# Optimization experiments

Hardware: AMD Instinct MI355X
Metric: run time of the kernel (lower is better)

## Reference

```python
import jax, jax.numpy as jnp
import numpy as np

B, T, D, H = 2, 2048, 1024, 16
DH = D // H


def setup_inputs() -> dict:
    key = jax.random.key(0)
    k1, k2, k3, k4 = jax.random.split(key, 4)
    x = jax.random.normal(k1, (B, T, D), dtype=jnp.float32)
    k = jax.random.normal(k2, (B, H, T, DH), dtype=jnp.float32)
    v = jax.random.normal(k3, (B, H, T, DH), dtype=jnp.float32)
    Wq = jax.random.normal(k4, (D, D), dtype=jnp.float32) * (1.0 / np.sqrt(D))
    return {"x": x, "k": k, "v": v, "Wq": Wq}


def reference(x, k, v, Wq):
    b, t, d = x.shape
    h = k.shape[1]
    scale = 1.0 / jnp.sqrt(jnp.float32(d))  # note: sqrt(d), NOT sqrt(d/h), per source
    # q = Linear(d, d, bias=False): y = x @ Wq.T, then split into heads
    q = jnp.einsum('btd,ed->bte', x, Wq).reshape(b, t, h, -1).transpose(0, 2, 1, 3)  # [b,h,t,dh]
    scores = jnp.einsum('bhqd,bhkd->bhqk', q, k) * scale  # [b,h,t,t]
    causal = jnp.triu(jnp.ones((t, t), dtype=bool), k=1)  # True above diagonal -> masked
    scores = jnp.where(causal[None, None], -jnp.inf, scores)
    a = jax.nn.softmax(scores, axis=-1)
    out = jnp.einsum('bhqk,bhkd->bhqd', a, v).transpose(0, 2, 1, 3).reshape(b, t, d)
    return x + out
```

## Files before the change

kernel.cpp:

```cpp
#include <hip/hip_runtime.h>
#include <hip/hip_bf16.h>

#define B_ 2
#define T_ 2048
#define D_ 1024
#define H_ 16
#define DH_ 64

typedef __attribute__((ext_vector_type(8))) short bf16x8;
typedef __attribute__((ext_vector_type(4))) short bf16x4;
typedef __attribute__((ext_vector_type(4))) float f32x4;
typedef __attribute__((ext_vector_type(8))) unsigned short u16x8;

__device__ __forceinline__ unsigned short f2bf(float f) {
    unsigned int u = __float_as_uint(f);
    return (unsigned short)((u + 0x7FFFu + ((u >> 16) & 1u)) >> 16);
}

__device__ __forceinline__ void pack8(const float4& a, const float4& b, u16x8& o) {
    o[0] = f2bf(a.x); o[1] = f2bf(a.y); o[2] = f2bf(a.z); o[3] = f2bf(a.w);
    o[4] = f2bf(b.x); o[5] = f2bf(b.y); o[6] = f2bf(b.z); o[7] = f2bf(b.w);
}

__device__ __forceinline__ f32x4 mfma16(bf16x4 a, bf16x4 b, f32x4 c) {
#if defined(__HIP_DEVICE_COMPILE__)
    return __builtin_amdgcn_mfma_f32_16x16x16bf16_1k(a, b, c, 0, 0, 0);
#else
    return c;
#endif
}

__global__ __launch_bounds__(256) void conv_kernel(
    const float* __restrict__ k, const float* __restrict__ v,
    unsigned short* __restrict__ kb, unsigned short* __restrict__ vt)
{
    __shared__ float Ts[64][65];
    const int tid = threadIdx.x;
    const int bi = blockIdx.x;

    if (bi < 512) {
        const float* src = k + ((size_t)bi * 256 + tid) * 32;
        unsigned short* dst = kb + ((size_t)bi * 256 + tid) * 32;
        #pragma unroll
        for (int u = 0; u < 4; ++u) {
            const float4 a = *(const float4*)(src + u * 8);
            const float4 b = *(const float4*)(src + u * 8 + 4);
            u16x8 o; pack8(a, b, o);
            *(u16x8*)(dst + u * 8) = o;
        }
        return;
    }

    const int idx = bi - 512;
    const int t0 = (idx & 31) * 64;
    const int hb = idx >> 5;
    const size_t bh = (size_t)(hb >> 4) * H_ + (hb & 15);
    #pragma unroll
    for (int u = 0; u < 4; ++u) {
        const int tr = u * 16 + (tid >> 4);
        const int dc = (tid & 15) * 4;
        const float4 r = *(const float4*)(v + (bh * T_ + t0 + tr) * DH_ + dc);
        Ts[tr][dc + 0] = r.x; Ts[tr][dc + 1] = r.y;
        Ts[tr][dc + 2] = r.z; Ts[tr][dc + 3] = r.w;
    }
    __syncthreads();
    #pragma unroll
    for (int u = 0; u < 4; ++u) {
        const int dh = u * 16 + (tid >> 4);
        const int tc = (tid & 15) * 4;
        ushort4 o;
        o.x = f2bf(Ts[tc + 0][dh]); o.y = f2bf(Ts[tc + 1][dh]);
        o.z = f2bf(Ts[tc + 2][dh]); o.w = f2bf(Ts[tc + 3][dh]);
        *(ushort4*)(vt + (bh * DH_ + dh) * T_ + t0 + tc) = o;
    }
}

__global__ __launch_bounds__(256, 4) void mega_attn(
    const float* __restrict__ xg,
    const float* __restrict__ Wq,
    const unsigned short* __restrict__ kb,
    const unsigned short* __restrict__ vt,
    float* __restrict__ out)
{
    __shared__ __align__(16) char lds_raw[36864];
    unsigned short (*Ks0)[72] = (unsigned short(*)[72])(lds_raw);
    unsigned short (*Ks1)[72] = (unsigned short(*)[72])(lds_raw + 9216);
    unsigned short (*Vs0)[72] = (unsigned short(*)[72])(lds_raw + 18432);
    unsigned short (*Vs1)[72] = (unsigned short(*)[72])(lds_raw + 27648);
    unsigned short (*Ws)[72] = (unsigned short(*)[72])(lds_raw);
    unsigned short (*Xs)[72] = (unsigned short(*)[72])(lds_raw + 9216);
    unsigned short (*Qs)[72] = (unsigned short(*)[72])(lds_raw + 27648);

    const int tid = threadIdx.x;
    const int lane = tid & 63;
    const int w = tid >> 6;
    const int l15 = lane & 15, l4 = lane >> 4;
    const int bi = blockIdx.x;
    const int qt = 31 - (bi >> 5);
    const int hb = bi & 31;
    const int h = hb & 15, b = hb >> 4;
    const int q0 = qt * 64;
    const size_t bh = (size_t)b * H_ + h;

    {
        const int row = tid >> 2;
        const int cf  = (tid & 3) * 16;
        const float* xg0 = xg + ((size_t)b * T_ + q0 + row) * D_ + cf;
        const float* wg0 = Wq + (size_t)(h * 64 + row) * D_ + cf;

        f32x4 acc[4] = {};
        for (int k0 = 0; k0 < D_; k0 += 64) {
            {
                const float* g = xg0 + k0;
                u16x8 p0, p1;
                pack8(*(const float4*)(g), *(const float4*)(g + 4), p0);
                pack8(*(const float4*)(g + 8), *(const float4*)(g + 12), p1);
                *(u16x8*)&Xs[row][cf] = p0;
                *(u16x8*)&Xs[row][cf + 8] = p1;
                const float* gw = wg0 + k0;
                pack8(*(const float4*)(gw), *(const float4*)(gw + 4), p0);
                pack8(*(const float4*)(gw + 8), *(const float4*)(gw + 12), p1);
                *(u16x8*)&Ws[row][cf] = p0;
                *(u16x8*)&Ws[row][cf + 8] = p1;
            }
            __syncthreads();
            #pragma unroll
            for (int kc = 0; kc < 2; ++kc) {
                const bf16x8 wf = *(const bf16x8*)&Ws[w * 16 + l15][kc * 32 + l4 * 8];
                #pragma unroll
                for (int nt = 0; nt < 4; ++nt) {
                    const bf16x8 xf = *(const bf16x8*)&Xs[nt * 16 + l15][kc * 32 + l4 * 8];
                    acc[nt] = __builtin_amdgcn_mfma_f32_16x16x32_bf16(wf, xf, acc[nt], 0, 0, 0);
                }
            }
            __syncthreads();
        }
        const float qscale = 1.0f / 32.0f;
        #pragma unroll
        for (int nt = 0; nt < 4; ++nt) {
            ushort4 o;
            o.x = f2bf(acc[nt][0] * qscale); o.y = f2bf(acc[nt][1] * qscale);
            o.z = f2bf(acc[nt][2] * qscale); o.w = f2bf(acc[nt][3] * qscale);
            *(ushort4*)&Qs[nt * 16 + l15][w * 16 + l4 * 4] = o;
        }
    }
    __syncthreads();

    bf16x8 qf[2];
    #pragma unroll
    for (int kc = 0; kc < 2; ++kc)
        qf[kc] = *(const bf16x8*)&Qs[w * 16 + l15][kc * 32 + l4 * 8];

    f32x4 o_acc[4] = {};
    float m_i = -INFINITY, l_i = 0.0f;

    const int srow = tid >> 2;
    const int scol = (tid & 3) * 16;

    {
        const unsigned short* gk = kb + (bh * T_ + srow) * DH_ + scol;
        *(uint4*)&Ks0[srow][scol] = *(const uint4*)gk;
        *(uint4*)&Ks0[srow][scol + 8] = *(const uint4*)(gk + 8);
        const unsigned short* gv = vt + (bh * DH_ + srow) * T_ + scol;
        *(uint4*)&Vs0[srow][scol] = *(const uint4*)gv;
        *(uint4*)&Vs0[srow][scol + 8] = *(const uint4*)(gv + 8);
    }
    __syncthreads();

    int p = 0;
    for (int j0 = 0; j0 <= q0; j0 += 64) {
        unsigned short (*Ksp)[72] = p ? Ks1 : Ks0;
        unsigned short (*Vsp)[72] = p ? Vs1 : Vs0;
        unsigned short (*Ksn)[72] = p ? Ks0 : Ks1;
        unsigned short (*Vsn)[72] = p ? Vs0 : Vs1;

        const int jn = (j0 + 64 <= q0) ? j0 + 64 : 0;
        uint4 kr0, kr1, vr0, vr1;
        {
            const unsigned short* gk = kb + (bh * T_ + jn + srow) * DH_ + scol;
            kr0 = *(const uint4*)gk;
            kr1 = *(const uint4*)(gk + 8);
            const unsigned short* gv = vt + (bh * DH_ + srow) * T_ + jn + scol;
            vr0 = *(const uint4*)gv;
            vr1 = *(const uint4*)(gv + 8);
        }

        f32x4 st[4] = {};
        #pragma unroll
        for (int kc = 0; kc < 2; ++kc) {
            #pragma unroll
            for (int nt = 0; nt < 4; ++nt) {
                const bf16x8 kf = *(const bf16x8*)&Ksp[nt * 16 + l15][kc * 32 + l4 * 8];
                st[nt] = __builtin_amdgcn_mfma_f32_16x16x32_bf16(kf, qf[kc], st[nt], 0, 0, 0);
            }
        }

        if (j0 == q0) {
            const int thr = w * 16 + l15 - l4 * 4;
            #pragma unroll
            for (int nt = 0; nt < 4; ++nt)
                #pragma unroll
                for (int r = 0; r < 4; ++r)
                    if (nt * 16 + r > thr) st[nt][r] = -INFINITY;
        }

        float rm = -INFINITY;
        #pragma unroll
        for (int nt = 0; nt < 4; ++nt)
            #pragma unroll
            for (int r = 0; r < 4; ++r) rm = fmaxf(rm, st[nt][r]);
        rm = fmaxf(rm, __shfl_xor(rm, 16));
        rm = fmaxf(rm, __shfl_xor(rm, 32));
        const float mn = fmaxf(m_i, rm);
        const float alpha = __expf(m_i - mn);
        float rs = 0.0f;
        #pragma unroll
        for (int nt = 0; nt < 4; ++nt)
            #pragma unroll
            for (int r = 0; r < 4; ++r) {
                const float pv = __expf(st[nt][r] - mn);
                st[nt][r] = pv;
                rs += pv;
            }
        rs += __shfl_xor(rs, 16);
        rs += __shfl_xor(rs, 32);
        l_i = l_i * alpha + rs;
        m_i = mn;
        #pragma unroll
        for (int mt = 0; mt < 4; ++mt)
            #pragma unroll
            for (int r = 0; r < 4; ++r) o_acc[mt][r] *= alpha;

        bf16x4 pf[4];
        #pragma unroll
        for (int nt = 0; nt < 4; ++nt) {
            union { unsigned int u[2]; bf16x4 s; } cv;
            cv.u[0] = __builtin_amdgcn_perm(__float_as_uint(st[nt][1]),
                                            __float_as_uint(st[nt][0]), 0x07060302u);
            cv.u[1] = __builtin_amdgcn_perm(__float_as_uint(st[nt][3]),
                                            __float_as_uint(st[nt][2]), 0x07060302u);
            pf[nt] = cv.s;
        }

        #pragma unroll
        for (int c = 0; c < 4; ++c) {
            #pragma unroll
            for (int mt = 0; mt < 4; ++mt) {
                const bf16x4 vf = *(const bf16x4*)&Vsp[mt * 16 + l15][c * 16 + l4 * 4];
                o_acc[mt] = mfma16(vf, pf[c], o_acc[mt]);
            }
        }

        *(uint4*)&Ksn[srow][scol] = kr0;
        *(uint4*)&Ksn[srow][scol + 8] = kr1;
        *(uint4*)&Vsn[srow][scol] = vr0;
        *(uint4*)&Vsn[srow][scol + 8] = vr1;
        __syncthreads();
        p ^= 1;
    }

    const float inv = 1.0f / l_i;
    const int qrow = q0 + w * 16 + l15;
    #pragma unroll
    for (int mt = 0; mt < 4; ++mt) {
        #pragma unroll
        for (int r = 0; r < 4; ++r) {
            const int d = h * DH_ + mt * 16 + l4 * 4 + r;
            const size_t off = ((size_t)b * T_ + qrow) * D_ + d;
            out[off] = xg[off] + o_acc[mt][r] * inv;
        }
    }
}

extern "C" void kernel_launch(void* const* d_in, const int* in_sizes, int n_in,
                              void* d_out, int out_size, void* d_ws, size_t ws_size,
                              hipStream_t stream) {
    const float* x  = (const float*)d_in[0];
    const float* k  = (const float*)d_in[1];
    const float* v  = (const float*)d_in[2];
    const float* Wq = (const float*)d_in[3];
    float* out = (float*)d_out;

    const size_t NE = (size_t)B_ * H_ * T_ * DH_;
    unsigned short* kb = (unsigned short*)d_ws;
    unsigned short* vt = kb + NE;

    conv_kernel<<<1536, 256, 0, stream>>>(k, v, kb, vt);
    mega_attn<<<1024, 256, 0, stream>>>(x, Wq, kb, vt, out);
}
```

Baseline: 169.2 us.

## Pre-convert x and Wq to bf16 and double-buffer the Q projection loop

The preprocessing kernel now also converts x and Wq to bf16 in workspace, so the fused attention kernel loads half-width data for its Q projection and skips repeated fp32-to-bf16 conversion. Each Wq head slice is loaded by 32 blocks and each x row tile by 16, so converting once removes redundant conversion and fp32 traffic. The Q-projection k-loop becomes register-prefetched and double-buffered in LDS, with one barrier per iteration instead of two. The cost is an extra pass writing bf16 copies of x and Wq plus more workspace, and the conversion kernel grows.

```diff
diff --git a/kernel.cpp b/kernel.cpp
--- a/kernel.cpp
+++ b/kernel.cpp
@@ -32,15 +32,23 @@
 
 __global__ __launch_bounds__(256) void conv_kernel(
     const float* __restrict__ k, const float* __restrict__ v,
-    unsigned short* __restrict__ kb, unsigned short* __restrict__ vt)
+    const float* __restrict__ x, const float* __restrict__ Wq,
+    unsigned short* __restrict__ kb, unsigned short* __restrict__ vt,
+    unsigned short* __restrict__ xb, unsigned short* __restrict__ wqb)
 {
     __shared__ float Ts[64][65];
     const int tid = threadIdx.x;
     const int bi = blockIdx.x;
 
-    if (bi < 512) {
-        const float* src = k + ((size_t)bi * 256 + tid) * 32;
-        unsigned short* dst = kb + ((size_t)bi * 256 + tid) * 32;
+    if (bi < 1152) {
+        const float* src;
+        unsigned short* dst;
+        if (bi < 512)       { src = k  + ((size_t)bi * 256 + tid) * 32;
+                              dst = kb  + ((size_t)bi * 256 + tid) * 32; }
+        else if (bi < 1024) { src = x  + ((size_t)(bi - 512) * 256 + tid) * 32;
+                              dst = xb  + ((size_t)(bi - 512) * 256 + tid) * 32; }
+        else                { src = Wq + ((size_t)(bi - 1024) * 256 + tid) * 32;
+                              dst = wqb + ((size_t)(bi - 1024) * 256 + tid) * 32; }
         #pragma unroll
         for (int u = 0; u < 4; ++u) {
             const float4 a = *(const float4*)(src + u * 8);
@@ -51,7 +59,7 @@
         return;
     }
 
-    const int idx = bi - 512;
+    const int idx = bi - 1152;
     const int t0 = (idx & 31) * 64;
     const int hb = idx >> 5;
     const size_t bh = (size_t)(hb >> 4) * H_ + (hb & 15);
@@ -76,20 +84,23 @@
 }
 
 __global__ __launch_bounds__(256, 4) void mega_attn(
-    const float* __restrict__ xg,
-    const float* __restrict__ Wq,
+    const unsigned short* __restrict__ xb,
+    const unsigned short* __restrict__ wqb,
     const unsigned short* __restrict__ kb,
     const unsigned short* __restrict__ vt,
+    const float* __restrict__ xg,
     float* __restrict__ out)
 {
     __shared__ __align__(16) char lds_raw[36864];
+    unsigned short (*Ws0)[72] = (unsigned short(*)[72])(lds_raw);
+    unsigned short (*Xs0)[72] = (unsigned short(*)[72])(lds_raw + 9216);
+    unsigned short (*Ws1)[72] = (unsigned short(*)[72])(lds_raw + 18432);
+    unsigned short (*Xs1)[72] = (unsigned short(*)[72])(lds_raw + 27648);
+    unsigned short (*Qs)[72]  = (unsigned short(*)[72])(lds_raw + 27648);
     unsigned short (*Ks0)[72] = (unsigned short(*)[72])(lds_raw);
     unsigned short (*Ks1)[72] = (unsigned short(*)[72])(lds_raw + 9216);
     unsigned short (*Vs0)[72] = (unsigned short(*)[72])(lds_raw + 18432);
     unsigned short (*Vs1)[72] = (unsigned short(*)[72])(lds_raw + 27648);
-    unsigned short (*Ws)[72] = (unsigned short(*)[72])(lds_raw);
-    unsigned short (*Xs)[72] = (unsigned short(*)[72])(lds_raw + 9216);
-    unsigned short (*Qs)[72] = (unsigned short(*)[72])(lds_raw + 27648);
 
     const int tid = threadIdx.x;
     const int lane = tid & 63;
@@ -102,39 +113,59 @@
     const int q0 = qt * 64;
     const size_t bh = (size_t)b * H_ + h;
 
+    const int srow = tid >> 2;
+    const int scol = (tid & 3) * 16;
+
+    f32x4 acc[4] = {};
     {
-        const int row = tid >> 2;
-        const int cf  = (tid & 3) * 16;
-        const float* xg0 = xg + ((size_t)b * T_ + q0 + row) * D_ + cf;
-        const float* wg0 = Wq + (size_t)(h * 64 + row) * D_ + cf;
-
-        f32x4 acc[4] = {};
-        for (int k0 = 0; k0 < D_; k0 += 64) {
-            {
-                const float* g = xg0 + k0;
-                u16x8 p0, p1;
-                pack8(*(const float4*)(g), *(const float4*)(g + 4), p0);
-                pack8(*(const float4*)(g + 8), *(const float4*)(g + 12), p1);
-                *(u16x8*)&Xs[row][cf] = p0;
-                *(u16x8*)&Xs[row][cf + 8] = p1;
-                const float* gw = wg0 + k0;
-                pack8(*(const float4*)(gw), *(const float4*)(gw + 4), p0);
-                pack8(*(const float4*)(gw + 8), *(const float4*)(gw + 12), p1);
-                *(u16x8*)&Ws[row][cf] = p0;
-                *(u16x8*)&Ws[row][cf + 8] = p1;
-            }
-            __syncthreads();
+        const unsigned short* xg0 = xb  + ((size_t)b * T_ + q0 + srow) * D_ + scol;
+        const unsigned short* wg0 = wqb + (size_t)(h * 64 + srow) * D_ + scol;
+
+        uint4 xr0 = *(const uint4*)(xg0);
+        uint4 xr1 = *(const uint4*)(xg0 + 8);
+        uint4 wr0 = *(const uint4*)(wg0);
+        uint4 wr1 = *(const uint4*)(wg0 + 8);
+        *(uint4*)&Xs0[srow][scol] = xr0;
+        *(uint4*)&Xs0[srow][scol + 8] = xr1;
+        *(uint4*)&Ws0[srow][scol] = wr0;
+        *(uint4*)&Ws0[srow][scol + 8] = wr1;
+        __syncthreads();
+
+        int p = 0;
+        for (int it = 0; it < 16; ++it) {
+            if (it < 15) {
+                const int kk = (it + 1) * 64;
+                xr0 = *(const uint4*)(xg0 + kk);
+                xr1 = *(const uint4*)(xg0 + kk + 8);
+                wr0 = *(const uint4*)(wg0 + kk);
+                wr1 = *(const uint4*)(wg0 + kk + 8);
+            }
+            unsigned short (*Wp)[72] = p ? Ws1 : Ws0;
+            unsigned short (*Xp)[72] = p ? Xs1 : Xs0;
             #pragma unroll
             for (int kc = 0; kc < 2; ++kc) {
-                const bf16x8 wf = *(const bf16x8*)&Ws[w * 16 + l15][kc * 32 + l4 * 8];
+                const bf16x8 wf = *(const bf16x8*)&Wp[w * 16 + l15][kc * 32 + l4 * 8];
                 #pragma unroll
                 for (int nt = 0; nt < 4; ++nt) {
-                    const bf16x8 xf = *(const bf16x8*)&Xs[nt * 16 + l15][kc * 32 + l4 * 8];
+                    const bf16x8 xf = *(const bf16x8*)&Xp[nt * 16 + l15][kc * 32 + l4 * 8];
                     acc[nt] = __builtin_amdgcn_mfma_f32_16x16x32_bf16(wf, xf, acc[nt], 0, 0, 0);
                 }
             }
-            __syncthreads();
-        }
+            if (it < 15) {
+                unsigned short (*Wn)[72] = p ? Ws0 : Ws1;
+                unsigned short (*Xn)[72] = p ? Xs0 : Xs1;
+                *(uint4*)&Xn[srow][scol] = xr0;
+                *(uint4*)&Xn[srow][scol + 8] = xr1;
+                *(uint4*)&Wn[srow][scol] = wr0;
+                *(uint4*)&Wn[srow][scol + 8] = wr1;
+                __syncthreads();
+                p ^= 1;
+            }
+        }
+    }
+    __syncthreads();
+
+    {
         const float qscale = 1.0f / 32.0f;
         #pragma unroll
         for (int nt = 0; nt < 4; ++nt) {
@@ -153,9 +184,6 @@
 
     f32x4 o_acc[4] = {};
     float m_i = -INFINITY, l_i = 0.0f;
-
-    const int srow = tid >> 2;
-    const int scol = (tid & 3) * 16;
 
     {
         const unsigned short* gk = kb + (bh * T_ + srow) * DH_ + scol;
@@ -282,9 +310,11 @@
     float* out = (float*)d_out;
 
     const size_t NE = (size_t)B_ * H_ * T_ * DH_;
-    unsigned short* kb = (unsigned short*)d_ws;
-    unsigned short* vt = kb + NE;
-
-    conv_kernel<<<1536, 256, 0, stream>>>(k, v, kb, vt);
-    mega_attn<<<1024, 256, 0, stream>>>(x, Wq, kb, vt, out);
-}
+    unsigned short* kb  = (unsigned short*)d_ws;
+    unsigned short* vt  = kb + NE;
+    unsigned short* xb  = vt + NE;
+    unsigned short* wqb = xb + NE;
+
+    conv_kernel<<<2176, 256, 0, stream>>>(k, v, x, Wq, kb, vt, xb, wqb);
+    mega_attn<<<1024, 256, 0, stream>>>(xb, wqb, kb, vt, x, out);
+}
```

Result: faster. 156.9 us (-7.3%).
